# Optimization experiments

Measured on AMD Instinct MI355X. Metric: run time of the kernel, lower is better.

Reference implementation:

```python
import jax, jax.numpy as jnp
import numpy as np

E = 1024   # embed_dim
H = 16     # num_heads
Dh = E // H
FF = 4 * E
LN_EPS = 1e-5


def _layernorm(x, g, b):
    mu = jnp.mean(x, axis=-1, keepdims=True)
    var = jnp.var(x, axis=-1, keepdims=True)
    return (x - mu) * jax.lax.rsqrt(var + LN_EPS) * g + b


def setup_inputs() -> dict:
    key = jax.random.key(0)
    ks = jax.random.split(key, 10)
    s = lambda fan_in: 1.0 / np.sqrt(fan_in)
    x = jax.random.normal(ks[0], (2, 2048, E), dtype=jnp.float32)
    Wq = jax.random.uniform(ks[1], (H, E, Dh), jnp.float32, -s(E), s(E))
    Wk = jax.random.uniform(ks[2], (H, E, Dh), jnp.float32, -s(E), s(E))
    Wproj = jax.random.uniform(ks[3], (E, E), jnp.float32, -s(E), s(E))
    bproj = jax.random.uniform(ks[4], (E,), jnp.float32, -s(E), s(E))
    ln1_g = jnp.ones((E,), jnp.float32)
    ln1_b = jnp.zeros((E,), jnp.float32)
    ln2_g = jnp.ones((E,), jnp.float32)
    ln2_b = jnp.zeros((E,), jnp.float32)
    W1 = jax.random.uniform(ks[5], (E, FF), jnp.float32, -s(E), s(E))
    b1 = jax.random.uniform(ks[6], (FF,), jnp.float32, -s(E), s(E))
    W2 = jax.random.uniform(ks[7], (FF, E), jnp.float32, -s(FF), s(FF))
    b2 = jax.random.uniform(ks[8], (E,), jnp.float32, -s(FF), s(FF))
    return dict(x=x, Wq=Wq, Wk=Wk, Wproj=Wproj, bproj=bproj,
                ln1_g=ln1_g, ln1_b=ln1_b, ln2_g=ln2_g, ln2_b=ln2_b,
                W1=W1, b1=b1, W2=W2, b2=b2)


def reference(x, Wq, Wk, Wproj, bproj, ln1_g, ln1_b, ln2_g, ln2_b, W1, b1, W2, b2):
    B, S, _ = x.shape
    # --- self-attention branch ---
    h = _layernorm(x, ln1_g, ln1_b)
    Q = jnp.einsum('bse,hed->bhsd', h, Wq)
    K = jnp.einsum('bse,hed->bhsd', h, Wk)
    # NOTE: original code uses V = key(x), so values == keys (faithful bug).
    scores = jnp.einsum('bhqd,bhkd->bhqk', Q, K) * (1.0 / np.sqrt(Dh))
    causal = jnp.tril(jnp.ones((S, S), dtype=bool))
    scores = jnp.where(causal, scores, -jnp.inf)
    attn = jax.nn.softmax(scores, axis=-1)  # dropout is identity in eval
    out = jnp.einsum('bhqk,bhkd->bhqd', attn, K)
    out = out.transpose(0, 2, 1, 3).reshape(B, S, H * Dh)
    x = x + out @ Wproj + bproj
    # --- MLP branch ---
    h2 = _layernorm(x, ln2_g, ln2_b)
    ff = jax.nn.relu(h2 @ W1 + b1) @ W2 + b2
    return x + ff
```

## Files before the change

### kernel.cpp

```cpp
#include <hip/hip_runtime.h>
#include <stdint.h>

typedef __bf16 bf16x8 __attribute__((ext_vector_type(8)));
typedef float f32x4 __attribute__((ext_vector_type(4)));
typedef float f32x16 __attribute__((ext_vector_type(16)));
typedef unsigned short u16;
typedef unsigned int u32;
typedef unsigned int u32x2 __attribute__((ext_vector_type(2)));

__device__ __forceinline__ u16 f2bf(float f) {
    u32 u = __builtin_bit_cast(u32, f);
    u = (u + 0x7fffu + ((u >> 16) & 1u)) >> 16;
    return (u16)u;
}
__device__ __forceinline__ float bf2f(u16 x) {
    return __builtin_bit_cast(float, (u32)x << 16);
}
__device__ __forceinline__ float fexp2(float x) {
#if __has_builtin(__builtin_amdgcn_exp2f)
    return __builtin_amdgcn_exp2f(x);
#else
    return exp2f(x);
#endif
}
__device__ __forceinline__ void plswap(u32& a, u32& b) {
#if __has_builtin(__builtin_amdgcn_permlane32_swap)
    u32x2 r = __builtin_amdgcn_permlane32_swap(a, b, false, false);
    a = r[0]; b = r[1];
#else
    asm volatile("v_permlane32_swap_b32 %0, %1" : "+v"(a), "+v"(b));
#endif
}

__device__ __forceinline__ void gload16(const u16* g, u16* l) {
    __builtin_amdgcn_global_load_lds(
        (const __attribute__((address_space(1))) unsigned int*)g,
        (__attribute__((address_space(3))) unsigned int*)l,
        16, 0, 0);
}

__device__ __constant__ unsigned char QB2[72] = {
    0,1,2,2,3,3,4,4,4,5,5,5,6,6,6,6,7,7,7,7,
    8,8,8,8,8,9,9,9,9,9,10,10,10,10,10,10,11,11,11,11,11,11,
    12,12,12,12,12,12,12,13,13,13,13,13,13,13,
    14,14,14,14,14,14,14,14,15,15,15,15,15,15,15,15};
__device__ __constant__ unsigned char CH2[72] = {
    0,0,0,1,0,1,0,1,2,0,1,2,0,1,2,3,0,1,2,3,
    0,1,2,3,4,0,1,2,3,4,0,1,2,3,4,5,0,1,2,3,4,5,
    0,1,2,3,4,5,6,0,1,2,3,4,5,6,
    0,1,2,3,4,5,6,7,0,1,2,3,4,5,6,7};
__device__ __constant__ unsigned char CUM2[17] =
    {0,1,2,4,6,9,12,16,20,25,30,36,42,49,56,64,72};

__global__ __launch_bounds__(256)
void prep_all(const float* __restrict__ Wq, const float* __restrict__ Wk,
              const float* __restrict__ Wproj, const float* __restrict__ W1,
              const float* __restrict__ W2,
              u16* __restrict__ wqkT, u16* __restrict__ wprojT,
              u16* __restrict__ w1T, u16* __restrict__ w2T,
              const float* __restrict__ x, const float* __restrict__ g1,
              const float* __restrict__ b1v, u16* __restrict__ hbuf) {
    __shared__ u16 tile[64 * 64];
    __shared__ float red[8];
    const int bid = blockIdx.x;
    const int t = threadIdx.x;
    if (bid >= 2816) {
        const int row = bid - 2816;
        float4 v = reinterpret_cast<const float4*>(x + (size_t)row * 1024)[t];
        float s = v.x + v.y + v.z + v.w;
        float sq = v.x * v.x + v.y * v.y + v.z * v.z + v.w * v.w;
        for (int o = 32; o > 0; o >>= 1) { s += __shfl_down(s, o); sq += __shfl_down(sq, o); }
        if ((t & 63) == 0) { red[t >> 6] = s; red[4 + (t >> 6)] = sq; }
        __syncthreads();
        float S  = red[0] + red[1] + red[2] + red[3];
        float SQ = red[4] + red[5] + red[6] + red[7];
        float mean = S * (1.f / 1024.f);
        float var  = SQ * (1.f / 1024.f) - mean * mean;
        float rstd = rsqrtf(var + 1e-5f);
        float4 g4 = reinterpret_cast<const float4*>(g1)[t];
        float4 b4 = reinterpret_cast<const float4*>(b1v)[t];
        ushort4 o;
        o.x = f2bf((v.x - mean) * rstd * g4.x + b4.x);
        o.y = f2bf((v.y - mean) * rstd * g4.y + b4.y);
        o.z = f2bf((v.z - mean) * rstd * g4.z + b4.z);
        o.w = f2bf((v.w - mean) * rstd * g4.w + b4.w);
        reinterpret_cast<ushort4*>(hbuf + (size_t)row * 1024)[t] = o;
        return;
    }
    const float* src; u16* dst; int R, C, c0, r0; size_t zb = 0;
    if (bid < 512) {
        const int q = bid & 255; const int z = q >> 4;
        src = (bid < 256) ? Wq : Wk;
        dst = (bid < 256) ? wqkT : (wqkT + 1048576);
        R = 1024; C = 64; c0 = 0; r0 = (q & 15) * 64; zb = (size_t)z * 65536;
    } else if (bid < 768) {
        const int q = bid - 512; src = Wproj; dst = wprojT; R = 1024; C = 1024;
        c0 = (q & 15) * 64; r0 = (q >> 4) * 64;
    } else if (bid < 1792) {
        const int q = bid - 768; src = W1; dst = w1T; R = 1024; C = 4096;
        c0 = (q & 63) * 64; r0 = (q >> 6) * 64;
    } else {
        const int q = bid - 1792; src = W2; dst = w2T; R = 4096; C = 1024;
        c0 = (q & 15) * 64; r0 = (q >> 4) * 64;
    }
    {
        const int r = t >> 2, j4 = t & 3;
        #pragma unroll
        for (int j = 0; j < 4; ++j) {
            int c = j4 * 4 + j * 16;
            float4 v = *reinterpret_cast<const float4*>(src + zb + (size_t)(r0 + r) * C + c0 + c);
            tile[(c + 0) * 64 + (r ^ (((c + 0) & 7) * 8))] = f2bf(v.x);
            tile[(c + 1) * 64 + (r ^ (((c + 1) & 7) * 8))] = f2bf(v.y);
            tile[(c + 2) * 64 + (r ^ (((c + 2) & 7) * 8))] = f2bf(v.z);
            tile[(c + 3) * 64 + (r ^ (((c + 3) & 7) * 8))] = f2bf(v.w);
        }
    }
    __syncthreads();
    {
        const int cc = t >> 2, j4 = t & 3;
        const int sw = (cc & 7) * 8;
        #pragma unroll
        for (int j2 = 0; j2 < 4; ++j2) {
            int rbase = j4 * 16 + j2 * 4;
            ushort4 o;
            o.x = tile[cc * 64 + ((rbase + 0) ^ sw)];
            o.y = tile[cc * 64 + ((rbase + 1) ^ sw)];
            o.z = tile[cc * 64 + ((rbase + 2) ^ sw)];
            o.w = tile[cc * 64 + ((rbase + 3) ^ sw)];
            *reinterpret_cast<ushort4*>(dst + zb + (size_t)(c0 + cc) * R + r0 + rbase) = o;
        }
    }
}

__global__ __launch_bounds__(256)
void ln_kernel(const float* __restrict__ x, u16* __restrict__ out,
               const float* __restrict__ gw, const float* __restrict__ bw) {
    __shared__ float red[8];
    int row = blockIdx.x, t = threadIdx.x;
    float4 v = reinterpret_cast<const float4*>(x + (size_t)row * 1024)[t];
    float s = v.x + v.y + v.z + v.w;
    float sq = v.x * v.x + v.y * v.y + v.z * v.z + v.w * v.w;
    for (int o = 32; o > 0; o >>= 1) { s += __shfl_down(s, o); sq += __shfl_down(sq, o); }
    if ((t & 63) == 0) { red[t >> 6] = s; red[4 + (t >> 6)] = sq; }
    __syncthreads();
    float S  = red[0] + red[1] + red[2] + red[3];
    float SQ = red[4] + red[5] + red[6] + red[7];
    float mean = S * (1.f / 1024.f);
    float var  = SQ * (1.f / 1024.f) - mean * mean;
    float rstd = rsqrtf(var + 1e-5f);
    float4 g4 = reinterpret_cast<const float4*>(gw)[t];
    float4 b4 = reinterpret_cast<const float4*>(bw)[t];
    ushort4 o;
    o.x = f2bf((v.x - mean) * rstd * g4.x + b4.x);
    o.y = f2bf((v.y - mean) * rstd * g4.y + b4.y);
    o.z = f2bf((v.z - mean) * rstd * g4.z + b4.z);
    o.w = f2bf((v.w - mean) * rstd * g4.w + b4.w);
    reinterpret_cast<ushort4*>(out + (size_t)row * 1024)[t] = o;
}

__global__ __launch_bounds__(256)
void ln2red_kernel(const float4* __restrict__ p0, const float4* __restrict__ p1,
                   const float4* __restrict__ x4, const float* __restrict__ bproj,
                   const float* __restrict__ gw, const float* __restrict__ bw,
                   float4* __restrict__ xmid, u16* __restrict__ out) {
    __shared__ float red[8];
    const int row = blockIdx.x, t = threadIdx.x;
    const size_t idx = (size_t)row * 256 + t;
    float4 a = p0[idx], b = p1[idx], xx = x4[idx];
    const float4 bp = *reinterpret_cast<const float4*>(bproj + (t << 2));
    float4 v;
    v.x = a.x + b.x + xx.x + bp.x;
    v.y = a.y + b.y + xx.y + bp.y;
    v.z = a.z + b.z + xx.z + bp.z;
    v.w = a.w + b.w + xx.w + bp.w;
    xmid[idx] = v;
    float s = v.x + v.y + v.z + v.w;
    float sq = v.x * v.x + v.y * v.y + v.z * v.z + v.w * v.w;
    for (int o = 32; o > 0; o >>= 1) { s += __shfl_down(s, o); sq += __shfl_down(sq, o); }
    if ((t & 63) == 0) { red[t >> 6] = s; red[4 + (t >> 6)] = sq; }
    __syncthreads();
    float S  = red[0] + red[1] + red[2] + red[3];
    float SQ = red[4] + red[5] + red[6] + red[7];
    float mean = S * (1.f / 1024.f);
    float var  = SQ * (1.f / 1024.f) - mean * mean;
    float rstd = rsqrtf(var + 1e-5f);
    const float4 g4 = *reinterpret_cast<const float4*>(gw + (t << 2));
    const float4 b4 = *reinterpret_cast<const float4*>(bw + (t << 2));
    ushort4 o;
    o.x = f2bf((v.x - mean) * rstd * g4.x + b4.x);
    o.y = f2bf((v.y - mean) * rstd * g4.y + b4.y);
    o.z = f2bf((v.z - mean) * rstd * g4.z + b4.z);
    o.w = f2bf((v.w - mean) * rstd * g4.w + b4.w);
    *reinterpret_cast<ushort4*>(out + idx * 4) = o;
}

template<int EPI, typename OT>
__global__ __launch_bounds__(256)
void gemm_bt(const u16* __restrict__ A, const u16* __restrict__ B,
             OT* __restrict__ C, const float* __restrict__ bias,
             const float* __restrict__ res, int K, int N, u16* __restrict__ ktr) {
    __shared__ u16 Al[128 * 64];
    __shared__ u16 Bl[128 * 64];
    const int t = threadIdx.x;
    const int lane = t & 63;
    const int w = t >> 6;
    const int wm = w >> 1, wn = w & 1;
    const int l15 = lane & 15, gq = lane >> 4;
    const int gx = gridDim.x;
    const int nwg = gx * gridDim.y;
    const int bid = blockIdx.y * gx + blockIdx.x;
    const int sw = ((nwg & 7) == 0) ? ((bid & 7) * (nwg >> 3) + (bid >> 3)) : bid;
    const int col0 = (sw % gx) * 128;
    const int row0 = (sw / gx) * 128;

    f32x4 acc[4][4] = {};

    const int nkb = K >> 6;
    for (int kb = 0; kb < nkb; ++kb) {
        #pragma unroll
        for (int i = 0; i < 4; ++i) {
            int slot = i * 256 + t;
            int r = slot >> 3;
            int g = (slot & 7) ^ (r & 7);
            gload16(A + (size_t)(row0 + r) * K + kb * 64 + g * 8, Al + slot * 8);
            gload16(B + (size_t)(col0 + r) * K + kb * 64 + g * 8, Bl + slot * 8);
        }
        __syncthreads();
        #pragma unroll
        for (int s = 0; s < 2; ++s) {
            bf16x8 af[4], bfr[4];
            #pragma unroll
            for (int mi = 0; mi < 4; ++mi) {
                int rl = wm * 64 + mi * 16 + l15;
                int ba = rl * 128 + ((s * 64 + gq * 16) ^ ((rl & 7) << 4));
                af[mi] = *reinterpret_cast<const bf16x8*>(reinterpret_cast<const char*>(Al) + ba);
            }
            #pragma unroll
            for (int ni = 0; ni < 4; ++ni) {
                int rl = wn * 64 + ni * 16 + l15;
                int ba = rl * 128 + ((s * 64 + gq * 16) ^ ((rl & 7) << 4));
                bfr[ni] = *reinterpret_cast<const bf16x8*>(reinterpret_cast<const char*>(Bl) + ba);
            }
            #pragma unroll
            for (int mi = 0; mi < 4; ++mi)
                #pragma unroll
                for (int ni = 0; ni < 4; ++ni)
                    acc[mi][ni] = __builtin_amdgcn_mfma_f32_16x16x32_bf16(af[mi], bfr[ni], acc[mi][ni], 0, 0, 0);
        }
        __syncthreads();
    }

    #pragma unroll
    for (int mi = 0; mi < 4; ++mi) {
        #pragma unroll
        for (int ni = 0; ni < 4; ++ni) {
            int gcol = col0 + wn * 64 + ni * 16 + l15;
            int grow0 = row0 + wm * 64 + mi * 16 + gq * 4;
            #pragma unroll
            for (int r = 0; r < 4; ++r) {
                int grow = grow0 + r;
                float v = acc[mi][ni][r];
                if constexpr (EPI == 1 || EPI == 2) v += bias[gcol];
                if constexpr (EPI == 1) v += res[(size_t)grow * N + gcol];
                if constexpr (EPI == 2) v = fmaxf(v, 0.f);
                if constexpr (sizeof(OT) == 4) C[(size_t)grow * N + gcol] = v;
                else                           C[(size_t)grow * N + gcol] = f2bf(v);
            }
        }
    }
}

#define DS_A(MH) \
  _Pragma("unroll") \
  for (int mi = 0; mi < 4; ++mi) { \
    const int rl = wm * 128 + (MH) * 64 + mi * 16 + l15; \
    const char* rp = abase + rl * 128; \
    const int sw2 = (rl & 7) << 4; \
    af[mi][0] = *reinterpret_cast<const bf16x8*>(rp + ((gq * 16) ^ sw2)); \
    af[mi][1] = *reinterpret_cast<const bf16x8*>(rp + ((64 + gq * 16) ^ sw2)); \
  }

#define DS_B(NH) \
  _Pragma("unroll") \
  for (int ni = 0; ni < 2; ++ni) { \
    const int rl = wn * 64 + (NH) * 32 + ni * 16 + l15; \
    const char* rp = bbase + rl * 128; \
    const int sw2 = (rl & 7) << 4; \
    bfr[ni][0] = *reinterpret_cast<const bf16x8*>(rp + ((gq * 16) ^ sw2)); \
    bfr[ni][1] = *reinterpret_cast<const bf16x8*>(rp + ((64 + gq * 16) ^ sw2)); \
  }

#define ST_A(HALF, KP, DB) \
  _Pragma("unroll") \
  for (int i = 0; i < 2; ++i) { \
    const int idx = i * 512 + t; const int rs = idx >> 3; const int kc = idx & 7; \
    const int row = (rs & 63) + ((rs >> 6) << 7) + (HALF) * 64; \
    gload16(Ag + (size_t)(row0 + row) * Kf + (KP) + ((kc ^ (row & 7)) << 3), (DB) + row * 64 + kc * 8); \
  }

#define ST_B(HALF, KP, DB) \
  _Pragma("unroll") \
  for (int i = 0; i < 2; ++i) { \
    const int idx = i * 512 + t; const int rs = idx >> 3; const int kc = idx & 7; \
    const int row = (rs & 31) + ((rs >> 5) << 6) + (HALF) * 32; \
    gload16(Bg + (size_t)(col0 + row) * Kf + (KP) + ((kc ^ (row & 7)) << 3), (DB) + row * 64 + kc * 8); \
  }

#define MFMA_Q(MH, NH) \
  _Pragma("unroll") \
  for (int mi = 0; mi < 4; ++mi) { \
    _Pragma("unroll") \
    for (int ni = 0; ni < 2; ++ni) { \
      acc[MH][mi][NH][ni] = __builtin_amdgcn_mfma_f32_16x16x32_bf16(af[mi][0], bfr[ni][0], acc[MH][mi][NH][ni], 0, 0, 0); \
      acc[MH][mi][NH][ni] = __builtin_amdgcn_mfma_f32_16x16x32_bf16(af[mi][1], bfr[ni][1], acc[MH][mi][NH][ni], 0, 0, 0); \
    } \
  }

#define WAITV(N) asm volatile("s_waitcnt vmcnt(" #N ")" ::: "memory")
#define BAR() __builtin_amdgcn_s_barrier()
#define PRIO1() __builtin_amdgcn_s_setprio(1)
#define PRIO0() __builtin_amdgcn_s_setprio(0)

template<int EPI, typename OT>
__global__ __launch_bounds__(512, 2)
void gemm256(const u16* __restrict__ A, const u16* __restrict__ B, OT* __restrict__ C,
             const float* __restrict__ bias, const float* __restrict__ res,
             int Kf, int KC, int N, u16* __restrict__ ktr) {
    __shared__ u16 AL[2][16384];
    __shared__ u16 BL[2][16384];
    const int t = threadIdx.x;
    const int lane = t & 63;
    const int w = t >> 6;
    const int wm = w >> 2, wn = w & 3;
    const int l15 = lane & 15, gq = lane >> 4;
    const int gx = gridDim.x;
    const int nwg = gx * gridDim.y;
    const int bid = blockIdx.y * gx + blockIdx.x;
    const int sw = ((nwg & 7) == 0) ? ((bid & 7) * (nwg >> 3) + (bid >> 3)) : bid;
    const int col0 = (sw % gx) * 256;
    const int row0 = (sw / gx) * 256;
    const int kbase = blockIdx.z * KC;
    const u16* Ag = A;
    const u16* Bg = B;

    f32x4 acc[2][4][2][2] = {};
    bf16x8 af[4][2], bfr[2][2];

    const int NT = KC >> 6;
    { u16* An = &AL[0][0]; u16* Bn = &BL[0][0];
      ST_A(0, kbase, An); ST_B(0, kbase, Bn); ST_B(1, kbase, Bn); ST_A(1, kbase, An); }
    WAITV(4);
    BAR();

    for (int tI = 0; tI < NT - 1; ++tI) {
        const int c = tI & 1;
        const char* abase = reinterpret_cast<const char*>(&AL[c][0]);
        const char* bbase = reinterpret_cast<const char*>(&BL[c][0]);
        u16* An = &AL[c ^ 1][0];
        u16* Bn = &BL[c ^ 1][0];
        const int kn = kbase + (tI + 1) * 64;
        DS_A(0); DS_B(0);
        ST_A(0, kn, An);
        WAITV(4); BAR();
        PRIO1(); MFMA_Q(0, 0); PRIO0();
        BAR();
        DS_B(1);
        ST_B(0, kn, Bn);
        WAITV(4); BAR();
        PRIO1(); MFMA_Q(0, 1); PRIO0();
        BAR();
        DS_A(1); DS_B(0);
        ST_B(1, kn, Bn);
        BAR();
        PRIO1(); MFMA_Q(1, 0); PRIO0();
        BAR();
        DS_B(1);
        ST_A(1, kn, An);
        WAITV(4); BAR();
        PRIO1(); MFMA_Q(1, 1); PRIO0();
        BAR();
    }
    {
        const int c = (NT - 1) & 1;
        const char* abase = reinterpret_cast<const char*>(&AL[c][0]);
        const char* bbase = reinterpret_cast<const char*>(&BL[c][0]);
        DS_A(0); DS_B(0);
        WAITV(2); BAR();
        PRIO1(); MFMA_Q(0, 0); PRIO0();
        BAR();
        DS_B(1);
        WAITV(0); BAR();
        PRIO1(); MFMA_Q(0, 1); PRIO0();
        BAR();
        DS_A(1); DS_B(0);
        BAR();
        PRIO1(); MFMA_Q(1, 0); PRIO0();
        BAR();
        DS_B(1);
        PRIO1(); MFMA_Q(1, 1); PRIO0();
    }

    const size_t Crow0 = (size_t)blockIdx.z * ((size_t)gridDim.y * 256);
    #pragma unroll
    for (int mh = 0; mh < 2; ++mh)
    #pragma unroll
    for (int mi = 0; mi < 4; ++mi)
    #pragma unroll
    for (int nh = 0; nh < 2; ++nh)
    #pragma unroll
    for (int ni = 0; ni < 2; ++ni) {
        const int gcol = col0 + wn * 64 + nh * 32 + ni * 16 + l15;
        const int grow0 = row0 + wm * 128 + mh * 64 + mi * 16 + gq * 4;
        f32x4 v = acc[mh][mi][nh][ni];
        if constexpr (EPI == 2) {
            const float bb = bias[gcol];
            v[0] += bb; v[1] += bb; v[2] += bb; v[3] += bb;
        }
        #pragma unroll
        for (int r = 0; r < 4; ++r) {
            const size_t o = (Crow0 + grow0 + r) * N + gcol;
            float x = v[r];
            if constexpr (EPI == 2) x = fmaxf(x, 0.f);
            if constexpr (sizeof(OT) == 4) C[o] = x;
            else                           C[o] = f2bf(x);
        }
    }
}

#define DS_B2 \
  _Pragma("unroll") \
  for (int ni = 0; ni < 2; ++ni) { \
    const int rl = wn * 32 + ni * 16 + l15; \
    const char* rp = bbase + rl * 128; \
    const int sw2 = (rl & 7) << 4; \
    bfr[ni][0] = *reinterpret_cast<const bf16x8*>(rp + ((gq * 16) ^ sw2)); \
    bfr[ni][1] = *reinterpret_cast<const bf16x8*>(rp + ((64 + gq * 16) ^ sw2)); \
  }

#define ST_B2(KP, DB) \
  _Pragma("unroll") \
  for (int i = 0; i < 2; ++i) { \
    const int idx = i * 512 + t; const int rs = idx >> 3; const int kc = idx & 7; \
    gload16(Bg + (size_t)(col0 + rs) * Kf + (KP) + ((kc ^ (rs & 7)) << 3), (DB) + rs * 64 + kc * 8); \
  }

#define MFMA_Q2(MH) \
  _Pragma("unroll") \
  for (int mi = 0; mi < 4; ++mi) { \
    _Pragma("unroll") \
    for (int ni = 0; ni < 2; ++ni) { \
      acc[MH][mi][ni] = __builtin_amdgcn_mfma_f32_16x16x32_bf16(af[mi][0], bfr[ni][0], acc[MH][mi][ni], 0, 0, 0); \
      acc[MH][mi][ni] = __builtin_amdgcn_mfma_f32_16x16x32_bf16(af[mi][1], bfr[ni][1], acc[MH][mi][ni], 0, 0, 0); \
    } \
  }

template<int EPI, typename OT>
__global__ __launch_bounds__(512, 2)
void gemmN128(const u16* __restrict__ A, const u16* __restrict__ B, OT* __restrict__ C,
              int Kf, int KC, int N, u16* __restrict__ ktr) {
    __shared__ u16 AL[2][16384];
    __shared__ u16 BL[2][8192];
    const int t = threadIdx.x;
    const int lane = t & 63;
    const int w = t >> 6;
    const int wm = w >> 2, wn = w & 3;
    const int l15 = lane & 15, gq = lane >> 4;
    const int gx = gridDim.x;
    const int nwg = gx * gridDim.y;
    const int bid = blockIdx.y * gx + blockIdx.x;
    const int sw = ((nwg & 7) == 0) ? ((bid & 7) * (nwg >> 3) + (bid >> 3)) : bid;
    const int col0 = (sw % gx) * 128;
    const int row0 = (sw / gx) * 256;
    const int kbase = blockIdx.z * KC;
    const u16* Ag = A;
    const u16* Bg = B;

    f32x4 acc[2][4][2] = {};
    bf16x8 af[4][2], bfr[2][2];

    const int NT = KC >> 6;
    { u16* An = &AL[0][0]; u16* Bn = &BL[0][0];
      ST_A(0, kbase, An); ST_B2(kbase, Bn); ST_A(1, kbase, An); }
    WAITV(0);
    BAR();

    for (int tI = 0; tI < NT - 1; ++tI) {
        const int c = tI & 1;
        const char* abase = reinterpret_cast<const char*>(&AL[c][0]);
        const char* bbase = reinterpret_cast<const char*>(&BL[c][0]);
        u16* An = &AL[c ^ 1][0];
        u16* Bn = &BL[c ^ 1][0];
        const int kn = kbase + (tI + 1) * 64;
        DS_A(0); DS_B2;
        ST_A(0, kn, An); ST_B2(kn, Bn);
        WAITV(4); BAR();
        PRIO1(); MFMA_Q2(0); PRIO0();
        BAR();
        DS_A(1);
        ST_A(1, kn, An);
        WAITV(2); BAR();
        PRIO1(); MFMA_Q2(1); PRIO0();
        BAR();
    }
    {
        const int c = (NT - 1) & 1;
        const char* abase = reinterpret_cast<const char*>(&AL[c][0]);
        const char* bbase = reinterpret_cast<const char*>(&BL[c][0]);
        DS_A(0); DS_B2;
        WAITV(0); BAR();
        PRIO1(); MFMA_Q2(0); PRIO0();
        BAR();
        DS_A(1);
        PRIO1(); MFMA_Q2(1); PRIO0();
    }

    const size_t Crow0 = (size_t)blockIdx.z * ((size_t)gridDim.y * 256);
    #pragma unroll
    for (int mh = 0; mh < 2; ++mh)
    #pragma unroll
    for (int mi = 0; mi < 4; ++mi)
    #pragma unroll
    for (int ni = 0; ni < 2; ++ni) {
        const int gcol = col0 + wn * 32 + ni * 16 + l15;
        const int grow0 = row0 + wm * 128 + mh * 64 + mi * 16 + gq * 4;
        f32x4 v = acc[mh][mi][ni];
        if constexpr (EPI == 3) {
            if (gcol < 1024) {
                const float QS = 0.18033688f;
                v[0] *= QS; v[1] *= QS; v[2] *= QS; v[3] *= QS;
            }
        }
        #pragma unroll
        for (int r = 0; r < 4; ++r) {
            const size_t o = (Crow0 + grow0 + r) * N + gcol;
            if constexpr (sizeof(OT) == 4) C[o] = v[r];
            else                           C[o] = f2bf(v[r]);
        }
        if constexpr (EPI == 3) {
            if (gcol >= 1024) {
                ushort4 k4;
                k4.x = f2bf(v[0]); k4.y = f2bf(v[1]); k4.z = f2bf(v[2]); k4.w = f2bf(v[3]);
                *reinterpret_cast<ushort4*>(ktr + (size_t)(gcol - 1024) * 4096 + grow0) = k4;
            }
        }
    }
}

__global__ __launch_bounds__(256)
void reduce2_kernel(const float4* __restrict__ p0, const float4* __restrict__ p1,
                    const float4* __restrict__ xm, const float* __restrict__ b2,
                    float4* __restrict__ out) {
    const int i = blockIdx.x * 256 + threadIdx.x;
    float4 a = p0[i], b = p1[i], x = xm[i];
    const float4 bb = *reinterpret_cast<const float4*>(b2 + ((i & 255) << 2));
    float4 o;
    o.x = x.x + bb.x + a.x + b.x;
    o.y = x.y + bb.y + a.y + b.y;
    o.z = x.z + bb.z + a.z + b.z;
    o.w = x.w + bb.w + a.w + b.w;
    out[i] = o;
}

template<int SPLIT>
__global__ __launch_bounds__(256)
void attn_kernel(const u16* __restrict__ qk, const u16* __restrict__ ktr, u16* __restrict__ out,
                 u16* __restrict__ pO, float* __restrict__ pl) {
    __shared__ u16 Kl[2][64 * 64];
    __shared__ u16 Tl[2][64 * 64];
    const int t = threadIdx.x;
    const int lane = t & 63;
    const int w = t >> 6;
    const int l31 = lane & 31, hi = lane >> 5;
    int bh, qb, npc, cid, s0, s1;
    if constexpr (SPLIT) {
        bh = blockIdx.x & 31;
        cid = blockIdx.x >> 5;
        qb = QB2[cid];
        const int ch = CH2[cid];
        npc = CUM2[qb + 1] - CUM2[qb];
        const int nt = 2 * (qb + 1);
        s0 = ch * 4;
        s1 = min(nt, s0 + 4);
    } else {
        bh = blockIdx.x & 31;
        const int tt = blockIdx.x >> 5;
        qb = (tt < 8) ? tt : 23 - tt;
        cid = 0; npc = 1; s0 = 0; s1 = 2 * (qb + 1);
    }
    const int b = bh >> 4, h = bh & 15;
    const int q0w = qb * 128 + w * 32;
    const int q = q0w + l31;
    const int qwmax = q0w + 31;
    const u16* Qp = qk + (size_t)b * 2048 * 2048 + h * 64;
    const u16* Kp = Qp + 1024;
    const u16* Tp = ktr + (size_t)h * 64 * 4096 + (size_t)b * 2048;

    bf16x8 qf[4];
    #pragma unroll
    for (int s = 0; s < 4; ++s)
        qf[s] = *reinterpret_cast<const bf16x8*>(Qp + (size_t)q * 2048 + s * 16 + hi * 8);

    f32x16 oacc[2] = {};
    float lsum = 0.f;

    {
        #pragma unroll
        for (int i = 0; i < 2; ++i) {
            int slot = i * 256 + t;
            int r = slot >> 3;
            int g = (slot & 7) ^ (r & 7);
            gload16(Kp + (size_t)(s0 * 64 + r) * 2048 + g * 8, &Kl[0][0] + slot * 8);
            gload16(Tp + (size_t)r * 4096 + s0 * 64 + g * 8, &Tl[0][0] + slot * 8);
        }
    }

    for (int kt = s0; kt < s1; ++kt) {
        const int cur = (kt - s0) & 1;
        __syncthreads();
        if (kt + 1 < s1) {
            int k0 = (kt + 1) * 64;
            #pragma unroll
            for (int i = 0; i < 2; ++i) {
                int slot = i * 256 + t;
                int r = slot >> 3;
                int g = (slot & 7) ^ (r & 7);
                gload16(Kp + (size_t)(k0 + r) * 2048 + g * 8, &Kl[cur ^ 1][0] + slot * 8);
                gload16(Tp + (size_t)r * 4096 + k0 + g * 8, &Tl[cur ^ 1][0] + slot * 8);
            }
        }
        const int kbase = kt * 64;
        if (kbase > qwmax) continue;
        const u16* kl = &Kl[cur][0];
        const u16* tl = &Tl[cur][0];

        f32x16 st0 = {}, st1 = {};
        PRIO1();
        #pragma unroll
        for (int s = 0; s < 4; ++s) {
            {
                int r = l31;
                int col = (16 * s + 8 * hi) ^ ((r & 7) * 8);
                bf16x8 kf = *reinterpret_cast<const bf16x8*>(kl + r * 64 + col);
                st0 = __builtin_amdgcn_mfma_f32_32x32x16_bf16(kf, qf[s], st0, 0, 0, 0);
            }
            {
                int r = 32 + l31;
                int col = (16 * s + 8 * hi) ^ ((r & 7) * 8);
                bf16x8 kf = *reinterpret_cast<const bf16x8*>(kl + r * 64 + col);
                st1 = __builtin_amdgcn_mfma_f32_32x32x16_bf16(kf, qf[s], st1, 0, 0, 0);
            }
        }
        PRIO0();

        float p[32];
        if (kbase + 63 <= q0w) {
            #pragma unroll
            for (int i = 0; i < 16; ++i) { p[i] = st0[i]; p[16 + i] = st1[i]; }
        } else {
            #pragma unroll
            for (int i = 0; i < 16; ++i) {
                int kloc = kbase + (i & 3) + 8 * (i >> 2) + 4 * hi;
                p[i]      = (kloc      <= q) ? st0[i] : -3.0e38f;
                p[16 + i] = (kloc + 32 <= q) ? st1[i] : -3.0e38f;
            }
        }
        #pragma unroll
        for (int i = 0; i < 32; ++i) p[i] = fexp2(p[i]);
        float s0v = 0.f, s1v = 0.f, s2v = 0.f, s3v = 0.f;
        #pragma unroll
        for (int i = 0; i < 8; ++i) {
            s0v += p[4 * i]; s1v += p[4 * i + 1]; s2v += p[4 * i + 2]; s3v += p[4 * i + 3];
        }
        lsum += (s0v + s1v) + (s2v + s3v);

        u32 wds[16];
        #pragma unroll
        for (int j = 0; j < 16; ++j) {
            u16 a = __builtin_bit_cast(u16, (__bf16)p[2 * j]);
            u16 c = __builtin_bit_cast(u16, (__bf16)p[2 * j + 1]);
            wds[j] = (u32)a | ((u32)c << 16);
        }
        union PF { u32 wd[4]; bf16x8 b; } pf[4];
        #pragma unroll
        for (int qd = 0; qd < 4; ++qd) {
            u32 a = wds[4 * qd + 0], bb = wds[4 * qd + 2];
            u32 c = wds[4 * qd + 1], d = wds[4 * qd + 3];
            plswap(a, bb);
            plswap(c, d);
            pf[qd].wd[0] = a; pf[qd].wd[1] = c; pf[qd].wd[2] = bb; pf[qd].wd[3] = d;
        }
        PRIO1();
        #pragma unroll
        for (int kc = 0; kc < 4; ++kc) {
            #pragma unroll
            for (int db = 0; db < 2; ++db) {
                int r = db * 32 + l31;
                int col = (kc * 16 + 8 * hi) ^ ((r & 7) * 8);
                bf16x8 vf = *reinterpret_cast<const bf16x8*>(tl + r * 64 + col);
                oacc[db] = __builtin_amdgcn_mfma_f32_32x32x16_bf16(vf, pf[kc].b, oacc[db], 0, 0, 0);
            }
        }
        PRIO0();
    }

    lsum += __shfl_xor(lsum, 32);

    if (npc == 1) {
        const float inv = 1.f / lsum;
        u16* op = out + (size_t)(b * 2048 + q) * 1024 + h * 64;
        #pragma unroll
        for (int db = 0; db < 2; ++db) {
            #pragma unroll
            for (int tq = 0; tq < 4; ++tq) {
                ushort4 o;
                o.x = f2bf(oacc[db][tq * 4 + 0] * inv);
                o.y = f2bf(oacc[db][tq * 4 + 1] * inv);
                o.z = f2bf(oacc[db][tq * 4 + 2] * inv);
                o.w = f2bf(oacc[db][tq * 4 + 3] * inv);
                *reinterpret_cast<ushort4*>(op + db * 32 + tq * 8 + hi * 4) = o;
            }
        }
    } else {
        const size_t g = (size_t)bh * 72 + cid;
        u16* po = pO + (g * 128 + (w * 32 + l31)) * 64;
        #pragma unroll
        for (int db = 0; db < 2; ++db) {
            #pragma unroll
            for (int tq = 0; tq < 4; ++tq) {
                ushort4 o;
                o.x = f2bf(oacc[db][tq * 4 + 0]);
                o.y = f2bf(oacc[db][tq * 4 + 1]);
                o.z = f2bf(oacc[db][tq * 4 + 2]);
                o.w = f2bf(oacc[db][tq * 4 + 3]);
                *reinterpret_cast<ushort4*>(po + db * 32 + tq * 8 + hi * 4) = o;
            }
        }
        if (hi == 0)
            pl[g * 128 + w * 32 + l31] = lsum;
    }
}

__global__ __launch_bounds__(256)
void attn_combine(const u16* __restrict__ pO, const float* __restrict__ pl,
                  u16* __restrict__ out) {
    const int g = blockIdx.x;
    const int bh = g & 31;
    const int qb = 2 + (g >> 5);
    const int b = bh >> 4, h = bh & 15;
    const int base = bh * 72 + CUM2[qb];
    const int npc = CUM2[qb + 1] - CUM2[qb];
    const int t = threadIdx.x;
    const int q = t >> 1;
    const int dh = (t & 1) << 5;

    float L = 0.f;
    float o[32] = {};
    for (int p = 0; p < 8; ++p) {
        if (p >= npc) break;
        L += pl[(size_t)(base + p) * 128 + q];
        const u16* src = pO + ((size_t)(base + p) * 128 + q) * 64 + dh;
        #pragma unroll
        for (int j = 0; j < 8; ++j) {
            ushort4 v = *reinterpret_cast<const ushort4*>(src + j * 4);
            o[4 * j + 0] += bf2f(v.x);
            o[4 * j + 1] += bf2f(v.y);
            o[4 * j + 2] += bf2f(v.z);
            o[4 * j + 3] += bf2f(v.w);
        }
    }
    const float inv = 1.f / L;
    u16* dst = out + ((size_t)(b * 2048 + qb * 128 + q)) * 1024 + h * 64 + dh;
    #pragma unroll
    for (int j = 0; j < 8; ++j) {
        ushort4 w4;
        w4.x = f2bf(o[4 * j + 0] * inv);
        w4.y = f2bf(o[4 * j + 1] * inv);
        w4.z = f2bf(o[4 * j + 2] * inv);
        w4.w = f2bf(o[4 * j + 3] * inv);
        *reinterpret_cast<ushort4*>(dst + j * 4) = w4;
    }
}

extern "C" void kernel_launch(void* const* d_in, const int* in_sizes, int n_in,
                              void* d_out, int out_size, void* d_ws, size_t ws_size,
                              hipStream_t stream) {
    const float* x     = (const float*)d_in[0];
    const float* Wq    = (const float*)d_in[1];
    const float* Wk    = (const float*)d_in[2];
    const float* Wproj = (const float*)d_in[3];
    const float* bproj = (const float*)d_in[4];
    const float* ln1g  = (const float*)d_in[5];
    const float* ln1b  = (const float*)d_in[6];
    const float* ln2g  = (const float*)d_in[7];
    const float* ln2b  = (const float*)d_in[8];
    const float* W1    = (const float*)d_in[9];
    const float* b1    = (const float*)d_in[10];
    const float* W2    = (const float*)d_in[11];
    const float* b2    = (const float*)d_in[12];

    char* ws = (char*)d_ws;
    u16*   wqkT   = (u16*)(ws + 0);
    u16*   wprojT = (u16*)(ws + (4ull << 20));
    u16*   w1T    = (u16*)(ws + (6ull << 20));
    u16*   w2T    = (u16*)(ws + (14ull << 20));
    u16*   hbuf   = (u16*)(ws + (22ull << 20));
    float* xmid   = (float*)(ws + (30ull << 20));
    u16*   qk     = (u16*)(ws + (46ull << 20));
    u16*   ktr    = (u16*)(ws + (62ull << 20));
    u16*   attnb  = (u16*)(ws + (70ull << 20));
    u16*   ff     = (u16*)(ws + (46ull << 20));
    float* part   = (float*)(ws + (78ull << 20));
    u16*   pO16   = (u16*)(ws + (78ull << 20));
    float* pl     = (float*)(ws + (118ull << 20));
    const bool fast = ws_size >= (142ull << 20);

    prep_all<<<6912, 256, 0, stream>>>(Wq, Wk, Wproj, W1, W2,
                                       wqkT, wprojT, w1T, w2T,
                                       x, ln1g, ln1b, hbuf);
    gemmN128<3, u16><<<dim3(16, 16, 1), 512, 0, stream>>>(hbuf, wqkT, qk, 1024, 1024, 2048, ktr);
    if (fast) {
        attn_kernel<1><<<2304, 256, 0, stream>>>(qk, ktr, attnb, pO16, pl);
        attn_combine<<<448, 256, 0, stream>>>(pO16, pl, attnb);
    } else {
        attn_kernel<0><<<512, 256, 0, stream>>>(qk, ktr, attnb, nullptr, nullptr);
    }
    if (fast) {
        gemmN128<0, float><<<dim3(8, 16, 2), 512, 0, stream>>>(attnb, wprojT, part, 1024, 512, 1024, nullptr);
        ln2red_kernel<<<4096, 256, 0, stream>>>(
            (const float4*)part, (const float4*)(part + 4194304), (const float4*)x,
            bproj, ln2g, ln2b, (float4*)xmid, hbuf);
    } else {
        gemm_bt<1, float><<<dim3(8, 32), 256, 0, stream>>>(attnb, wprojT, xmid, bproj, x, 1024, 1024, nullptr);
        ln_kernel<<<4096, 256, 0, stream>>>(xmid, hbuf, ln2g, ln2b);
    }
    gemm256<2, u16><<<dim3(16, 16, 1), 512, 0, stream>>>(hbuf, w1T, ff, b1, nullptr, 1024, 1024, 4096, nullptr);
    if (fast) {
        gemmN128<0, float><<<dim3(8, 16, 2), 512, 0, stream>>>(ff, w2T, part, 4096, 2048, 1024, nullptr);
        reduce2_kernel<<<4096, 256, 0, stream>>>(
            (const float4*)part, (const float4*)(part + 4194304),
            (const float4*)xmid, b2, (float4*)d_out);
    } else {
        gemm_bt<1, float><<<dim3(8, 32), 256, 0, stream>>>(ff, w2T, (float*)d_out, b2, xmid, 4096, 1024, nullptr);
    }
}
```

Measured before the change: 213.2 us.

## Restructure GEMM prefetch into whole-tile issue and add XCD-aware block mapping

Both GEMM kernels now issue every global-to-LDS load for the next K tile at the start of each iteration. A single wait and barrier then precedes the four (or two) MFMA quarters, replacing the interleaved per-quarter loads and barriers. A new xcd_rect helper maps block IDs so the blocks on each XCD cover a compact rectangle of output tiles, aiming for better L2 reuse of A and B. The goal is fewer barriers and better cache locality, at the cost of less fine-grained overlap between loads and compute and a larger burst of outstanding memory traffic.

```diff
diff --git a/kernel.cpp b/kernel.cpp
--- a/kernel.cpp
+++ b/kernel.cpp
@@ -321,6 +321,21 @@
 #define PRIO1() __builtin_amdgcn_s_setprio(1)
 #define PRIO0() __builtin_amdgcn_s_setprio(0)
 
+__device__ __forceinline__ void xcd_rect(int bid, int gx, int nwg, int& colI, int& rowI) {
+    if (nwg == 256 && gx == 16) {
+        const int xcd = bid & 7, k = bid >> 3;
+        colI = (xcd & 3) * 4 + (k & 3);
+        rowI = (xcd >> 2) * 8 + (k >> 2);
+    } else if (nwg == 128 && gx == 8) {
+        const int xcd = bid & 7, k = bid >> 3;
+        colI = (xcd & 3) * 2 + (k & 1);
+        rowI = (xcd >> 2) * 8 + (k >> 1);
+    } else {
+        const int sw = ((nwg & 7) == 0) ? ((bid & 7) * (nwg >> 3) + (bid >> 3)) : bid;
+        colI = sw % gx; rowI = sw / gx;
+    }
+}
+
 template<int EPI, typename OT>
 __global__ __launch_bounds__(512, 2)
 void gemm256(const u16* __restrict__ A, const u16* __restrict__ B, OT* __restrict__ C,
@@ -336,9 +351,10 @@
     const int gx = gridDim.x;
     const int nwg = gx * gridDim.y;
     const int bid = blockIdx.y * gx + blockIdx.x;
-    const int sw = ((nwg & 7) == 0) ? ((bid & 7) * (nwg >> 3) + (bid >> 3)) : bid;
-    const int col0 = (sw % gx) * 256;
-    const int row0 = (sw / gx) * 256;
+    int colI, rowI;
+    xcd_rect(bid, gx, nwg, colI, rowI);
+    const int col0 = colI * 256;
+    const int row0 = rowI * 256;
     const int kbase = blockIdx.z * KC;
     const u16* Ag = A;
     const u16* Bg = B;
@@ -348,56 +364,31 @@
 
     const int NT = KC >> 6;
     { u16* An = &AL[0][0]; u16* Bn = &BL[0][0];
-      ST_A(0, kbase, An); ST_B(0, kbase, Bn); ST_B(1, kbase, Bn); ST_A(1, kbase, An); }
-    WAITV(4);
-    BAR();
-
-    for (int tI = 0; tI < NT - 1; ++tI) {
+      ST_A(0, kbase, An); ST_A(1, kbase, An); ST_B(0, kbase, Bn); ST_B(1, kbase, Bn); }
+
+    for (int tI = 0; tI < NT; ++tI) {
         const int c = tI & 1;
         const char* abase = reinterpret_cast<const char*>(&AL[c][0]);
         const char* bbase = reinterpret_cast<const char*>(&BL[c][0]);
-        u16* An = &AL[c ^ 1][0];
-        u16* Bn = &BL[c ^ 1][0];
-        const int kn = kbase + (tI + 1) * 64;
+        if (tI + 1 < NT) {
+            u16* An = &AL[c ^ 1][0];
+            u16* Bn = &BL[c ^ 1][0];
+            const int kn = kbase + (tI + 1) * 64;
+            ST_A(0, kn, An); ST_A(1, kn, An); ST_B(0, kn, Bn); ST_B(1, kn, Bn);
+            WAITV(8);
+        } else {
+            WAITV(0);
+        }
+        BAR();
         DS_A(0); DS_B(0);
-        ST_A(0, kn, An);
-        WAITV(4); BAR();
         PRIO1(); MFMA_Q(0, 0); PRIO0();
-        BAR();
         DS_B(1);
-        ST_B(0, kn, Bn);
-        WAITV(4); BAR();
         PRIO1(); MFMA_Q(0, 1); PRIO0();
-        BAR();
         DS_A(1); DS_B(0);
-        ST_B(1, kn, Bn);
-        BAR();
         PRIO1(); MFMA_Q(1, 0); PRIO0();
-        BAR();
         DS_B(1);
-        ST_A(1, kn, An);
-        WAITV(4); BAR();
         PRIO1(); MFMA_Q(1, 1); PRIO0();
         BAR();
-    }
-    {
-        const int c = (NT - 1) & 1;
-        const char* abase = reinterpret_cast<const char*>(&AL[c][0]);
-        const char* bbase = reinterpret_cast<const char*>(&BL[c][0]);
-        DS_A(0); DS_B(0);
-        WAITV(2); BAR();
-        PRIO1(); MFMA_Q(0, 0); PRIO0();
-        BAR();
-        DS_B(1);
-        WAITV(0); BAR();
-        PRIO1(); MFMA_Q(0, 1); PRIO0();
-        BAR();
-        DS_A(1); DS_B(0);
-        BAR();
-        PRIO1(); MFMA_Q(1, 0); PRIO0();
-        BAR();
-        DS_B(1);
-        PRIO1(); MFMA_Q(1, 1); PRIO0();
     }
 
     const size_t Crow0 = (size_t)blockIdx.z * ((size_t)gridDim.y * 256);
@@ -468,9 +459,10 @@
     const int gx = gridDim.x;
     const int nwg = gx * gridDim.y;
     const int bid = blockIdx.y * gx + blockIdx.x;
-    const int sw = ((nwg & 7) == 0) ? ((bid & 7) * (nwg >> 3) + (bid >> 3)) : bid;
-    const int col0 = (sw % gx) * 128;
-    const int row0 = (sw / gx) * 256;
+    int colI, rowI;
+    xcd_rect(bid, gx, nwg, colI, rowI);
+    const int col0 = colI * 128;
+    const int row0 = rowI * 256;
     const int kbase = blockIdx.z * KC;
     const u16* Ag = A;
     const u16* Bg = B;
@@ -480,38 +472,27 @@
 
     const int NT = KC >> 6;
     { u16* An = &AL[0][0]; u16* Bn = &BL[0][0];
-      ST_A(0, kbase, An); ST_B2(kbase, Bn); ST_A(1, kbase, An); }
-    WAITV(0);
-    BAR();
-
-    for (int tI = 0; tI < NT - 1; ++tI) {
+      ST_A(0, kbase, An); ST_A(1, kbase, An); ST_B2(kbase, Bn); }
+
+    for (int tI = 0; tI < NT; ++tI) {
         const int c = tI & 1;
         const char* abase = reinterpret_cast<const char*>(&AL[c][0]);
         const char* bbase = reinterpret_cast<const char*>(&BL[c][0]);
-        u16* An = &AL[c ^ 1][0];
-        u16* Bn = &BL[c ^ 1][0];
-        const int kn = kbase + (tI + 1) * 64;
+        if (tI + 1 < NT) {
+            u16* An = &AL[c ^ 1][0];
+            u16* Bn = &BL[c ^ 1][0];
+            const int kn = kbase + (tI + 1) * 64;
+            ST_A(0, kn, An); ST_A(1, kn, An); ST_B2(kn, Bn);
+            WAITV(6);
+        } else {
+            WAITV(0);
+        }
+        BAR();
         DS_A(0); DS_B2;
-        ST_A(0, kn, An); ST_B2(kn, Bn);
-        WAITV(4); BAR();
         PRIO1(); MFMA_Q2(0); PRIO0();
-        BAR();
         DS_A(1);
-        ST_A(1, kn, An);
-        WAITV(2); BAR();
         PRIO1(); MFMA_Q2(1); PRIO0();
         BAR();
-    }
-    {
-        const int c = (NT - 1) & 1;
-        const char* abase = reinterpret_cast<const char*>(&AL[c][0]);
-        const char* bbase = reinterpret_cast<const char*>(&BL[c][0]);
-        DS_A(0); DS_B2;
-        WAITV(0); BAR();
-        PRIO1(); MFMA_Q2(0); PRIO0();
-        BAR();
-        DS_A(1);
-        PRIO1(); MFMA_Q2(1); PRIO0();
     }
 
     const size_t Crow0 = (size_t)blockIdx.z * ((size_t)gridDim.y * 256);
```

Measured after the change: 230.0 us. +7.9%, slower.

## Keep both B fragment halves in registers and map workgroups to per-XCD rectangles

Applied to the files above, without the earlier changes.

The 256x256 GEMM now holds both N-halves of the B fragments in registers (bfr gains an NH dimension). The second M-half reuses them instead of reloading B from LDS, which removes two DS_B calls per k-tile. A new xcd_rect helper assigns each XCD a compact rectangle of output tiles for the 256- and 128-workgroup grid shapes, meant to improve L2 reuse of A and B rows and columns within an XCD. The extra bf16x8 registers raise VGPR pressure under launch_bounds(512,2), which risks spills.

```diff
diff --git a/kernel.cpp b/kernel.cpp
--- a/kernel.cpp
+++ b/kernel.cpp
@@ -286,8 +286,8 @@
     const int rl = wn * 64 + (NH) * 32 + ni * 16 + l15; \
     const char* rp = bbase + rl * 128; \
     const int sw2 = (rl & 7) << 4; \
-    bfr[ni][0] = *reinterpret_cast<const bf16x8*>(rp + ((gq * 16) ^ sw2)); \
-    bfr[ni][1] = *reinterpret_cast<const bf16x8*>(rp + ((64 + gq * 16) ^ sw2)); \
+    bfr[NH][ni][0] = *reinterpret_cast<const bf16x8*>(rp + ((gq * 16) ^ sw2)); \
+    bfr[NH][ni][1] = *reinterpret_cast<const bf16x8*>(rp + ((64 + gq * 16) ^ sw2)); \
   }
 
 #define ST_A(HALF, KP, DB) \
@@ -311,8 +311,8 @@
   for (int mi = 0; mi < 4; ++mi) { \
     _Pragma("unroll") \
     for (int ni = 0; ni < 2; ++ni) { \
-      acc[MH][mi][NH][ni] = __builtin_amdgcn_mfma_f32_16x16x32_bf16(af[mi][0], bfr[ni][0], acc[MH][mi][NH][ni], 0, 0, 0); \
-      acc[MH][mi][NH][ni] = __builtin_amdgcn_mfma_f32_16x16x32_bf16(af[mi][1], bfr[ni][1], acc[MH][mi][NH][ni], 0, 0, 0); \
+      acc[MH][mi][NH][ni] = __builtin_amdgcn_mfma_f32_16x16x32_bf16(af[mi][0], bfr[NH][ni][0], acc[MH][mi][NH][ni], 0, 0, 0); \
+      acc[MH][mi][NH][ni] = __builtin_amdgcn_mfma_f32_16x16x32_bf16(af[mi][1], bfr[NH][ni][1], acc[MH][mi][NH][ni], 0, 0, 0); \
     } \
   }
 
@@ -320,6 +320,21 @@
 #define BAR() __builtin_amdgcn_s_barrier()
 #define PRIO1() __builtin_amdgcn_s_setprio(1)
 #define PRIO0() __builtin_amdgcn_s_setprio(0)
+
+__device__ __forceinline__ void xcd_rect(int bid, int gx, int nwg, int& colI, int& rowI) {
+    if (nwg == 256 && gx == 16) {
+        const int xcd = bid & 7, k = bid >> 3;
+        colI = (xcd & 3) * 4 + (k & 3);
+        rowI = (xcd >> 2) * 8 + (k >> 2);
+    } else if (nwg == 128 && gx == 8) {
+        const int xcd = bid & 7, k = bid >> 3;
+        colI = (xcd & 3) * 2 + (k & 1);
+        rowI = (xcd >> 2) * 8 + (k >> 1);
+    } else {
+        const int sw = ((nwg & 7) == 0) ? ((bid & 7) * (nwg >> 3) + (bid >> 3)) : bid;
+        colI = sw % gx; rowI = sw / gx;
+    }
+}
 
 template<int EPI, typename OT>
 __global__ __launch_bounds__(512, 2)
@@ -336,15 +351,16 @@
     const int gx = gridDim.x;
     const int nwg = gx * gridDim.y;
     const int bid = blockIdx.y * gx + blockIdx.x;
-    const int sw = ((nwg & 7) == 0) ? ((bid & 7) * (nwg >> 3) + (bid >> 3)) : bid;
-    const int col0 = (sw % gx) * 256;
-    const int row0 = (sw / gx) * 256;
+    int colI, rowI;
+    xcd_rect(bid, gx, nwg, colI, rowI);
+    const int col0 = colI * 256;
+    const int row0 = rowI * 256;
     const int kbase = blockIdx.z * KC;
     const u16* Ag = A;
     const u16* Bg = B;
 
     f32x4 acc[2][4][2][2] = {};
-    bf16x8 af[4][2], bfr[2][2];
+    bf16x8 af[4][2], bfr[2][2][2];
 
     const int NT = KC >> 6;
     { u16* An = &AL[0][0]; u16* Bn = &BL[0][0];
@@ -369,12 +385,11 @@
         WAITV(4); BAR();
         PRIO1(); MFMA_Q(0, 1); PRIO0();
         BAR();
-        DS_A(1); DS_B(0);
+        DS_A(1);
         ST_B(1, kn, Bn);
         BAR();
         PRIO1(); MFMA_Q(1, 0); PRIO0();
         BAR();
-        DS_B(1);
         ST_A(1, kn, An);
         WAITV(4); BAR();
         PRIO1(); MFMA_Q(1, 1); PRIO0();
@@ -392,11 +407,10 @@
         WAITV(0); BAR();
         PRIO1(); MFMA_Q(0, 1); PRIO0();
         BAR();
-        DS_A(1); DS_B(0);
+        DS_A(1);
         BAR();
         PRIO1(); MFMA_Q(1, 0); PRIO0();
         BAR();
-        DS_B(1);
         PRIO1(); MFMA_Q(1, 1); PRIO0();
     }
 
@@ -468,9 +482,10 @@
     const int gx = gridDim.x;
     const int nwg = gx * gridDim.y;
     const int bid = blockIdx.y * gx + blockIdx.x;
-    const int sw = ((nwg & 7) == 0) ? ((bid & 7) * (nwg >> 3) + (bid >> 3)) : bid;
-    const int col0 = (sw % gx) * 128;
-    const int row0 = (sw / gx) * 256;
+    int colI, rowI;
+    xcd_rect(bid, gx, nwg, colI, rowI);
+    const int col0 = colI * 128;
+    const int row0 = rowI * 256;
     const int kbase = blockIdx.z * KC;
     const u16* Ag = A;
     const u16* Bg = B;
```

Result: no change. 214.4 us (+0.6%).
